# Kernel tuning notes

Hardware: AMD Instinct MI355X
Metric: run time of the kernel (lower is better)

## Reference

```python
import jax, jax.numpy as jnp
import numpy as np
from jax import lax

FORGET_BIAS = 1.0
EPS = 1e-12


def l2_normalize_time(x):
    # tf.nn.l2_normalize(x, dim=1): normalize over the timestep axis
    sq = jnp.sum(jnp.square(x), axis=1, keepdims=True)
    return x * lax.rsqrt(jnp.maximum(sq, EPS))


def lstm_layer(x, W, b, units):
    """TF LSTMCell: kernel (in+units, 4*units), gates split as i, j, f, o.
    x: [B, T, D] -> [B, T, units]"""
    B = x.shape[0]

    def step(carry, xt):
        c, h = carry
        z = jnp.concatenate([xt, h], axis=-1) @ W + b  # [B, 4*units]
        i, j, f, o = jnp.split(z, 4, axis=-1)
        c = jax.nn.sigmoid(f + FORGET_BIAS) * c + jax.nn.sigmoid(i) * jnp.tanh(j)
        h = jax.nn.sigmoid(o) * jnp.tanh(c)
        return (c, h), h

    init = (jnp.zeros((B, units), x.dtype), jnp.zeros((B, units), x.dtype))
    _, hs = lax.scan(step, init, jnp.swapaxes(x, 0, 1))  # [T, B, units]
    return jnp.swapaxes(hs, 0, 1)


def setup_inputs() -> dict:
    key = jax.random.key(0)
    ks = jax.random.split(key, 5)
    B, T, U = 256, 2048, 64
    x = jax.random.normal(ks[0], (B, T, 1), dtype=jnp.float32)
    # layer 0: LSTMCell(64), input dim 1 -> kernel (1+64, 4*64)
    W0 = jax.random.normal(ks[1], (1 + U, 4 * U), dtype=jnp.float32) * 0.05
    b0 = jnp.zeros((4 * U,), dtype=jnp.float32)
    # layer 1: LSTMCell(1), input dim 64 -> kernel (64+1, 4)
    W1 = jax.random.normal(ks[2], (U + 1, 4), dtype=jnp.float32) * 0.05
    b1 = jnp.zeros((4,), dtype=jnp.float32)
    # dense(1)
    Wd = jax.random.normal(ks[3], (1, 1), dtype=jnp.float32)
    bd = jnp.zeros((1,), dtype=jnp.float32)
    return {"x": x, "W0": W0, "b0": b0, "W1": W1, "b1": b1, "Wd": Wd, "bd": bd}


def reference(x, W0, b0, W1, b1, Wd, bd):
    h = l2_normalize_time(x)          # [B, T, 1]
    h = lstm_layer(h, W0, b0, 64)     # [B, T, 64]
    h = lstm_layer(h, W1, b1, 1)      # [B, T, 1]
    out = h @ Wd + bd                 # dense(1), no activation
    return out
```

## Files before the change

### kernel.cpp

```cpp
#include <hip/hip_runtime.h>
#include <math.h>

#define TT 2048
#define UU 64
#define BB 256
#define NTHR 192

typedef float v2f __attribute__((ext_vector_type(2)));
typedef float v4f __attribute__((ext_vector_type(4)));

__device__ __forceinline__ float frcp(float x) { return __builtin_amdgcn_rcpf(x); }
__device__ __forceinline__ float fsigmoid(float x) { return frcp(1.0f + __expf(-x)); }
__device__ __forceinline__ float ftanh(float x) { return 1.0f - 2.0f * frcp(1.0f + __expf(2.0f * x)); }

__device__ __forceinline__ void pkfma(v2f& a, v2f h, v2f w) {
    asm("v_pk_fma_f32 %0, %1, %2, %0" : "+v"(a) : "v"(h), "v"(w));
}

__global__
__attribute__((amdgpu_flat_work_group_size(NTHR, NTHR)))
__attribute__((amdgpu_waves_per_eu(1, 1)))
void lstm_ts_kernel(
    const float* __restrict__ x, const float* __restrict__ W0,
    const float* __restrict__ b0, const float* __restrict__ W1,
    const float* __restrict__ b1, const float* __restrict__ Wd,
    const float* __restrict__ bd, float* __restrict__ out)
{
    __shared__ __align__(16) float xbuf[TT];
    __shared__ __align__(16) float ringS0[2][2 * UU];
    __shared__ __align__(16) float ringS1[2][2 * UU];
    __shared__ __align__(16) v2f zb0[UU];
    __shared__ __align__(16) v2f zb1[UU];
    __shared__ float red[3];

    const int tid = threadIdx.x;
    const int wid = tid >> 6;
    const int u = tid & 63;
    const int b = blockIdx.x;
    const float* xrow = x + b * TT;
    float* outrow = out + b * TT;

    float ss = 0.f;
    for (int i = tid; i < TT; i += NTHR) {
        float v = xrow[i];
        xbuf[i] = v;
        ss += v * v;
    }
    #pragma unroll
    for (int m = 1; m < 64; m <<= 1) ss += __shfl_xor(ss, m, 64);
    if (u == 0) red[wid] = ss;
    if (wid < 2) {
        float* r1 = (wid == 0 ? ringS0 : ringS1)[1];
        r1[2 * u] = 0.f; r1[2 * u + 1] = 0.f;
    }
    __syncthreads();

    if (wid < 2) {
        const int go = wid * 128;
        const float sq = (red[0] + red[1]) + red[2];
        const float scale = 1.0f / sqrtf(fmaxf(sq, 1e-12f));

        #define DECLW(k) v2f WP##k; { const float* r_ = W0 + (1 + (k)) * 256 + go; \
            WP##k.x = r_[u]; WP##k.y = r_[64 + u]; } \
            asm volatile("" : "+v"(WP##k));
        DECLW(0)  DECLW(1)  DECLW(2)  DECLW(3)  DECLW(4)  DECLW(5)  DECLW(6)  DECLW(7)
        DECLW(8)  DECLW(9)  DECLW(10) DECLW(11) DECLW(12) DECLW(13) DECLW(14) DECLW(15)
        DECLW(16) DECLW(17) DECLW(18) DECLW(19) DECLW(20) DECLW(21) DECLW(22) DECLW(23)
        DECLW(24) DECLW(25) DECLW(26) DECLW(27) DECLW(28) DECLW(29) DECLW(30) DECLW(31)
        DECLW(32) DECLW(33) DECLW(34) DECLW(35) DECLW(36) DECLW(37) DECLW(38) DECLW(39)
        DECLW(40) DECLW(41) DECLW(42) DECLW(43) DECLW(44) DECLW(45) DECLW(46) DECLW(47)
        DECLW(48) DECLW(49) DECLW(50) DECLW(51) DECLW(52) DECLW(53) DECLW(54) DECLW(55)
        DECLW(56) DECLW(57) DECLW(58) DECLW(59) DECLW(60) DECLW(61) DECLW(62) DECLW(63)
        #undef DECLW

        const float wxa = W0[go + u] * scale;
        const float wxb = W0[go + 64 + u] * scale;
        const float bca = b0[go + u], bcb = b0[go + 64 + u];

        float (*myring)[2 * UU] = (wid == 0) ? ringS0 : ringS1;
        v2f* zbme = (wid == 0) ? zb0 : zb1;

        float c0 = 0.f;

        for (int t = 0; t < TT; ++t) {
            const float xr = xbuf[t];
            const float* hs = myring[(t + 1) & 1];

            v2f a0, a1 = 0.f, a2 = 0.f, a3 = 0.f;
            a0.x = fmaf(xr, wxa, bca); a0.y = fmaf(xr, wxb, bcb);

            #define MAC2(k2, Wa, Wb, Ae, Ao) { \
                v4f hv_ = *(const v4f*)(hs + 4 * (k2)); \
                v2f hlo_ = __builtin_shufflevector(hv_, hv_, 0, 1); \
                v2f hhi_ = __builtin_shufflevector(hv_, hv_, 2, 3); \
                pkfma(Ae, hlo_, Wa); pkfma(Ao, hhi_, Wb); \
            }
            MAC2(0,  WP0,  WP1,  a0, a1) MAC2(1,  WP2,  WP3,  a2, a3)
            MAC2(2,  WP4,  WP5,  a0, a1) MAC2(3,  WP6,  WP7,  a2, a3)
            MAC2(4,  WP8,  WP9,  a0, a1) MAC2(5,  WP10, WP11, a2, a3)
            MAC2(6,  WP12, WP13, a0, a1) MAC2(7,  WP14, WP15, a2, a3)
            MAC2(8,  WP16, WP17, a0, a1) MAC2(9,  WP18, WP19, a2, a3)
            MAC2(10, WP20, WP21, a0, a1) MAC2(11, WP22, WP23, a2, a3)
            MAC2(12, WP24, WP25, a0, a1) MAC2(13, WP26, WP27, a2, a3)
            MAC2(14, WP28, WP29, a0, a1) MAC2(15, WP30, WP31, a2, a3)
            MAC2(16, WP32, WP33, a0, a1) MAC2(17, WP34, WP35, a2, a3)
            MAC2(18, WP36, WP37, a0, a1) MAC2(19, WP38, WP39, a2, a3)
            MAC2(20, WP40, WP41, a0, a1) MAC2(21, WP42, WP43, a2, a3)
            MAC2(22, WP44, WP45, a0, a1) MAC2(23, WP46, WP47, a2, a3)
            MAC2(24, WP48, WP49, a0, a1) MAC2(25, WP50, WP51, a2, a3)
            MAC2(26, WP52, WP53, a0, a1) MAC2(27, WP54, WP55, a2, a3)
            MAC2(28, WP56, WP57, a0, a1) MAC2(29, WP58, WP59, a2, a3)
            MAC2(30, WP60, WP61, a0, a1) MAC2(31, WP62, WP63, a2, a3)
            #undef MAC2

            zbme[u] = (a0 + a1) + (a2 + a3);
            __syncthreads();

            const v2f zij = zb0[u];
            const v2f zfo = zb1[u];
            c0 = fsigmoid(zfo.x + 1.0f) * c0 + fsigmoid(zij.x) * ftanh(zij.y);
            const float h = fsigmoid(zfo.y) * ftanh(c0);

            v2f hh; hh.x = h; hh.y = h;
            *(v2f*)(&myring[t & 1][2 * u]) = hh;
        }
        __syncthreads();
    } else {
        const float w1v0 = W1[u * 4 + 0], w1v1 = W1[u * 4 + 1];
        const float w1v2 = W1[u * 4 + 2], w1v3 = W1[u * 4 + 3];
        const float w1h0 = W1[256], w1h1 = W1[257], w1h2 = W1[258], w1h3 = W1[259];
        const float b10 = b1[0], b11 = b1[1], b12 = b1[2], b13 = b1[3];
        const float wd = Wd[0], bdv = bd[0];

        float c1 = 0.f, h1 = 0.f, oval = 0.f;

        #define L1STEP(s) { \
            const float hu = ringS0[(s) & 1][2 * u];   \
            float p0 = hu * w1v0, p1 = hu * w1v1, p2 = hu * w1v2, p3 = hu * w1v3; \
            _Pragma("unroll") \
            for (int m = 1; m < 64; m <<= 1) { \
                p0 += __shfl_xor(p0, m, 64); \
                p1 += __shfl_xor(p1, m, 64); \
                p2 += __shfl_xor(p2, m, 64); \
                p3 += __shfl_xor(p3, m, 64); \
            } \
            const float z1i = p0 + fmaf(h1, w1h0, b10); \
            const float z1j = p1 + fmaf(h1, w1h1, b11); \
            const float z1f = p2 + fmaf(h1, w1h2, b12); \
            const float z1o = p3 + fmaf(h1, w1h3, b13); \
            c1 = fsigmoid(z1f + 1.0f) * c1 + fsigmoid(z1i) * ftanh(z1j); \
            h1 = fsigmoid(z1o) * ftanh(c1); \
            const float ov = fmaf(h1, wd, bdv); \
            if (((s) & 63) == u) oval = ov; \
            if (((s) & 63) == 63) outrow[((s) & ~63) + u] = oval; \
        }

        for (int t = 0; t < TT; ++t) {
            __syncthreads();
            if (t > 0) L1STEP(t - 1)
        }
        __syncthreads();
        L1STEP(TT - 1)
        #undef L1STEP
    }
}

extern "C" void kernel_launch(void* const* d_in, const int* in_sizes, int n_in,
                              void* d_out, int out_size, void* d_ws, size_t ws_size,
                              hipStream_t stream) {
    const float* x  = (const float*)d_in[0];
    const float* W0 = (const float*)d_in[1];
    const float* b0 = (const float*)d_in[2];
    const float* W1 = (const float*)d_in[3];
    const float* b1 = (const float*)d_in[4];
    const float* Wd = (const float*)d_in[5];
    const float* bd = (const float*)d_in[6];
    float* out = (float*)d_out;
    lstm_ts_kernel<<<BB, NTHR, 0, stream>>>(x, W0, b0, W1, b1, Wd, bd, out);
}
```

Before: 1.103 ms.

## Move half of recurrent weights to LDS and deepen h ring buffer

Keeps only the first 32 rows of each layer-0 wave's recurrent weights in registers, as 16 v4f. The other 32 rows are staged into a shared-memory array at kernel start and read as v4f every timestep. The h ring grows from two to four slots and the gate-exchange buffer is double-buffered. Each wave also keeps its own gate sums in registers instead of reloading them from shared memory. The aim is to cut register pressure and loosen hazards between the two layer waves, at the cost of 16 extra shared-memory loads per step on the serial recurrence path.

```diff
diff --git a/kernel.cpp b/kernel.cpp
--- a/kernel.cpp
+++ b/kernel.cpp
@@ -27,10 +27,9 @@
     const float* __restrict__ bd, float* __restrict__ out)
 {
     __shared__ __align__(16) float xbuf[TT];
-    __shared__ __align__(16) float ringS0[2][2 * UU];
-    __shared__ __align__(16) float ringS1[2][2 * UU];
-    __shared__ __align__(16) v2f zb0[UU];
-    __shared__ __align__(16) v2f zb1[UU];
+    __shared__ __align__(16) v4f  WL[2][16][UU];
+    __shared__ __align__(16) float ringP[2][4][2 * UU];
+    __shared__ __align__(16) v2f  zb[2][2][UU];
     __shared__ float red[3];
 
     const int tid = threadIdx.x;
@@ -46,12 +45,19 @@
         xbuf[i] = v;
         ss += v * v;
     }
+    for (int idx = tid; idx < 2 * 16 * UU; idx += NTHR) {
+        const int w = idx >> 10, m = (idx >> 6) & 15, uu = idx & 63;
+        const int base = (33 + 2 * m) * 256 + w * 128;
+        v4f e;
+        e.x = W0[base + uu];       e.y = W0[base + 64 + uu];
+        e.z = W0[base + 256 + uu]; e.w = W0[base + 256 + 64 + uu];
+        WL[w][m][uu] = e;
+    }
     #pragma unroll
     for (int m = 1; m < 64; m <<= 1) ss += __shfl_xor(ss, m, 64);
     if (u == 0) red[wid] = ss;
     if (wid < 2) {
-        float* r1 = (wid == 0 ? ringS0 : ringS1)[1];
-        r1[2 * u] = 0.f; r1[2 * u + 1] = 0.f;
+        ringP[wid][3][2 * u] = 0.f; ringP[wid][3][2 * u + 1] = 0.f;
     }
     __syncthreads();
 
@@ -60,69 +66,72 @@
         const float sq = (red[0] + red[1]) + red[2];
         const float scale = 1.0f / sqrtf(fmaxf(sq, 1e-12f));
 
-        #define DECLW(k) v2f WP##k; { const float* r_ = W0 + (1 + (k)) * 256 + go; \
-            WP##k.x = r_[u]; WP##k.y = r_[64 + u]; } \
-            asm volatile("" : "+v"(WP##k));
-        DECLW(0)  DECLW(1)  DECLW(2)  DECLW(3)  DECLW(4)  DECLW(5)  DECLW(6)  DECLW(7)
-        DECLW(8)  DECLW(9)  DECLW(10) DECLW(11) DECLW(12) DECLW(13) DECLW(14) DECLW(15)
-        DECLW(16) DECLW(17) DECLW(18) DECLW(19) DECLW(20) DECLW(21) DECLW(22) DECLW(23)
-        DECLW(24) DECLW(25) DECLW(26) DECLW(27) DECLW(28) DECLW(29) DECLW(30) DECLW(31)
-        DECLW(32) DECLW(33) DECLW(34) DECLW(35) DECLW(36) DECLW(37) DECLW(38) DECLW(39)
-        DECLW(40) DECLW(41) DECLW(42) DECLW(43) DECLW(44) DECLW(45) DECLW(46) DECLW(47)
-        DECLW(48) DECLW(49) DECLW(50) DECLW(51) DECLW(52) DECLW(53) DECLW(54) DECLW(55)
-        DECLW(56) DECLW(57) DECLW(58) DECLW(59) DECLW(60) DECLW(61) DECLW(62) DECLW(63)
-        #undef DECLW
+        #define DECLR(m) v4f R##m; { const float* r_ = W0 + (1 + 2*(m)) * 256 + go; \
+            R##m.x = r_[u]; R##m.y = r_[64 + u]; \
+            R##m.z = r_[256 + u]; R##m.w = r_[256 + 64 + u]; } \
+            asm volatile("" : "+v"(R##m));
+        DECLR(0)  DECLR(1)  DECLR(2)  DECLR(3)  DECLR(4)  DECLR(5)  DECLR(6)  DECLR(7)
+        DECLR(8)  DECLR(9)  DECLR(10) DECLR(11) DECLR(12) DECLR(13) DECLR(14) DECLR(15)
+        #undef DECLR
 
         const float wxa = W0[go + u] * scale;
         const float wxb = W0[go + 64 + u] * scale;
         const float bca = b0[go + u], bcb = b0[go + 64 + u];
 
-        float (*myring)[2 * UU] = (wid == 0) ? ringS0 : ringS1;
-        v2f* zbme = (wid == 0) ? zb0 : zb1;
-
+        float (*myring)[2 * UU] = ringP[wid];
+        const v4f* wl = &WL[wid][0][0];
         float c0 = 0.f;
 
         for (int t = 0; t < TT; ++t) {
             const float xr = xbuf[t];
-            const float* hs = myring[(t + 1) & 1];
+            const float* hs = myring[(t + 3) & 3];
 
             v2f a0, a1 = 0.f, a2 = 0.f, a3 = 0.f;
             a0.x = fmaf(xr, wxa, bca); a0.y = fmaf(xr, wxb, bcb);
 
-            #define MAC2(k2, Wa, Wb, Ae, Ao) { \
+            #define MACR(k2, R, Ae, Ao) { \
                 v4f hv_ = *(const v4f*)(hs + 4 * (k2)); \
                 v2f hlo_ = __builtin_shufflevector(hv_, hv_, 0, 1); \
                 v2f hhi_ = __builtin_shufflevector(hv_, hv_, 2, 3); \
-                pkfma(Ae, hlo_, Wa); pkfma(Ao, hhi_, Wb); \
+                pkfma(Ae, hlo_, __builtin_shufflevector(R, R, 0, 1)); \
+                pkfma(Ao, hhi_, __builtin_shufflevector(R, R, 2, 3)); \
             }
-            MAC2(0,  WP0,  WP1,  a0, a1) MAC2(1,  WP2,  WP3,  a2, a3)
-            MAC2(2,  WP4,  WP5,  a0, a1) MAC2(3,  WP6,  WP7,  a2, a3)
-            MAC2(4,  WP8,  WP9,  a0, a1) MAC2(5,  WP10, WP11, a2, a3)
-            MAC2(6,  WP12, WP13, a0, a1) MAC2(7,  WP14, WP15, a2, a3)
-            MAC2(8,  WP16, WP17, a0, a1) MAC2(9,  WP18, WP19, a2, a3)
-            MAC2(10, WP20, WP21, a0, a1) MAC2(11, WP22, WP23, a2, a3)
-            MAC2(12, WP24, WP25, a0, a1) MAC2(13, WP26, WP27, a2, a3)
-            MAC2(14, WP28, WP29, a0, a1) MAC2(15, WP30, WP31, a2, a3)
-            MAC2(16, WP32, WP33, a0, a1) MAC2(17, WP34, WP35, a2, a3)
-            MAC2(18, WP36, WP37, a0, a1) MAC2(19, WP38, WP39, a2, a3)
-            MAC2(20, WP40, WP41, a0, a1) MAC2(21, WP42, WP43, a2, a3)
-            MAC2(22, WP44, WP45, a0, a1) MAC2(23, WP46, WP47, a2, a3)
-            MAC2(24, WP48, WP49, a0, a1) MAC2(25, WP50, WP51, a2, a3)
-            MAC2(26, WP52, WP53, a0, a1) MAC2(27, WP54, WP55, a2, a3)
-            MAC2(28, WP56, WP57, a0, a1) MAC2(29, WP58, WP59, a2, a3)
-            MAC2(30, WP60, WP61, a0, a1) MAC2(31, WP62, WP63, a2, a3)
-            #undef MAC2
+            #define MACL(k2, Ae, Ao) { \
+                v4f Wv_ = wl[((k2) - 16) * UU + u]; \
+                MACR(k2, Wv_, Ae, Ao) \
+            }
+            MACR(0,  R0,  a0, a1) MACR(1,  R1,  a2, a3)
+            MACR(2,  R2,  a0, a1) MACR(3,  R3,  a2, a3)
+            MACR(4,  R4,  a0, a1) MACR(5,  R5,  a2, a3)
+            MACR(6,  R6,  a0, a1) MACR(7,  R7,  a2, a3)
+            MACR(8,  R8,  a0, a1) MACR(9,  R9,  a2, a3)
+            MACR(10, R10, a0, a1) MACR(11, R11, a2, a3)
+            MACR(12, R12, a0, a1) MACR(13, R13, a2, a3)
+            MACR(14, R14, a0, a1) MACR(15, R15, a2, a3)
+            MACL(16, a0, a1) MACL(17, a2, a3)
+            MACL(18, a0, a1) MACL(19, a2, a3)
+            MACL(20, a0, a1) MACL(21, a2, a3)
+            MACL(22, a0, a1) MACL(23, a2, a3)
+            MACL(24, a0, a1) MACL(25, a2, a3)
+            MACL(26, a0, a1) MACL(27, a2, a3)
+            MACL(28, a0, a1) MACL(29, a2, a3)
+            MACL(30, a0, a1) MACL(31, a2, a3)
+            #undef MACL
+            #undef MACR
 
-            zbme[u] = (a0 + a1) + (a2 + a3);
+            const v2f zown = (a0 + a1) + (a2 + a3);
+            zb[t & 1][wid][u] = zown;
             __syncthreads();
 
-            const v2f zij = zb0[u];
-            const v2f zfo = zb1[u];
+            const v2f zoth = zb[t & 1][1 - wid][u];
+            const v2f zij = (wid == 0) ? zown : zoth;
+            const v2f zfo = (wid == 0) ? zoth : zown;
+
             c0 = fsigmoid(zfo.x + 1.0f) * c0 + fsigmoid(zij.x) * ftanh(zij.y);
             const float h = fsigmoid(zfo.y) * ftanh(c0);
 
             v2f hh; hh.x = h; hh.y = h;
-            *(v2f*)(&myring[t & 1][2 * u]) = hh;
+            *(v2f*)(&myring[t & 3][2 * u]) = hh;
         }
         __syncthreads();
     } else {
@@ -135,7 +144,7 @@
         float c1 = 0.f, h1 = 0.f, oval = 0.f;
 
         #define L1STEP(s) { \
-            const float hu = ringS0[(s) & 1][2 * u];   \
+            const float hu = ringP[0][(s) & 3][2 * u];   \
             float p0 = hu * w1v0, p1 = hu * w1v1, p2 = hu * w1v2, p3 = hu * w1v3; \
             _Pragma("unroll") \
             for (int m = 1; m < 64; m <<= 1) { \
```

Measured after the change: 1.297 ms. 17.6% more time.

## Exchange LSTM gate halves via cross-lane shuffle instead of LDS

Applied to the files above, without the earlier changes.

Layer-0 work is remapped so each wave owns 32 hidden units. The two 32-lane halves of a wave compute the (i,j) and (f,o) gate pairs for the same unit, and they swap partial gate values with a lane-xor-32 shuffle. This removes the per-step LDS write and read of gate pre-activations through the zb buffers from the recurrent critical path, and the two per-wave h rings merge into one shared ring. The layer-1 wave now reads the current step's h right after the same barrier instead of lagging one step, which removes the epilogue step.

```diff
diff --git a/kernel.cpp b/kernel.cpp
--- a/kernel.cpp
+++ b/kernel.cpp
@@ -27,15 +27,12 @@
     const float* __restrict__ bd, float* __restrict__ out)
 {
     __shared__ __align__(16) float xbuf[TT];
-    __shared__ __align__(16) float ringS0[2][2 * UU];
-    __shared__ __align__(16) float ringS1[2][2 * UU];
-    __shared__ __align__(16) v2f zb0[UU];
-    __shared__ __align__(16) v2f zb1[UU];
+    __shared__ __align__(16) float ring[2][2 * UU];
     __shared__ float red[3];
 
     const int tid = threadIdx.x;
     const int wid = tid >> 6;
-    const int u = tid & 63;
+    const int l = tid & 63;
     const int b = blockIdx.x;
     const float* xrow = x + b * TT;
     float* outrow = out + b * TT;
@@ -48,20 +45,20 @@
     }
     #pragma unroll
     for (int m = 1; m < 64; m <<= 1) ss += __shfl_xor(ss, m, 64);
-    if (u == 0) red[wid] = ss;
-    if (wid < 2) {
-        float* r1 = (wid == 0 ? ringS0 : ringS1)[1];
-        r1[2 * u] = 0.f; r1[2 * u + 1] = 0.f;
-    }
+    if (l == 0) red[wid] = ss;
+    if (tid < 2 * UU) ring[1][tid] = 0.f;
     __syncthreads();
 
     if (wid < 2) {
-        const int go = wid * 128;
+        const int p = l >> 5;
+        const int q = l & 31;
+        const int unit = 32 * wid + q;
+        const int go = p * 128;
         const float sq = (red[0] + red[1]) + red[2];
         const float scale = 1.0f / sqrtf(fmaxf(sq, 1e-12f));
 
         #define DECLW(k) v2f WP##k; { const float* r_ = W0 + (1 + (k)) * 256 + go; \
-            WP##k.x = r_[u]; WP##k.y = r_[64 + u]; } \
+            WP##k.x = r_[unit]; WP##k.y = r_[64 + unit]; } \
             asm volatile("" : "+v"(WP##k));
         DECLW(0)  DECLW(1)  DECLW(2)  DECLW(3)  DECLW(4)  DECLW(5)  DECLW(6)  DECLW(7)
         DECLW(8)  DECLW(9)  DECLW(10) DECLW(11) DECLW(12) DECLW(13) DECLW(14) DECLW(15)
@@ -73,18 +70,15 @@
         DECLW(56) DECLW(57) DECLW(58) DECLW(59) DECLW(60) DECLW(61) DECLW(62) DECLW(63)
         #undef DECLW
 
-        const float wxa = W0[go + u] * scale;
-        const float wxb = W0[go + 64 + u] * scale;
-        const float bca = b0[go + u], bcb = b0[go + 64 + u];
-
-        float (*myring)[2 * UU] = (wid == 0) ? ringS0 : ringS1;
-        v2f* zbme = (wid == 0) ? zb0 : zb1;
+        const float wxa = W0[go + unit] * scale;
+        const float wxb = W0[go + 64 + unit] * scale;
+        const float bca = b0[go + unit], bcb = b0[go + 64 + unit];
 
         float c0 = 0.f;
 
         for (int t = 0; t < TT; ++t) {
             const float xr = xbuf[t];
-            const float* hs = myring[(t + 1) & 1];
+            const float* hs = ring[(t + 1) & 1];
 
             v2f a0, a1 = 0.f, a2 = 0.f, a3 = 0.f;
             a0.x = fmaf(xr, wxa, bca); a0.y = fmaf(xr, wxb, bcb);
@@ -113,55 +107,54 @@
             MAC2(30, WP60, WP61, a0, a1) MAC2(31, WP62, WP63, a2, a3)
             #undef MAC2
 
-            zbme[u] = (a0 + a1) + (a2 + a3);
+            const v2f zown = (a0 + a1) + (a2 + a3);
+
+            const float ox = __shfl_xor(zown.x, 32, 64);
+            const float oy = __shfl_xor(zown.y, 32, 64);
+            const float zi = p ? ox : zown.x;
+            const float zj = p ? oy : zown.y;
+            const float zf = p ? zown.x : ox;
+            const float zo = p ? zown.y : oy;
+
+            c0 = fsigmoid(zf + 1.0f) * c0 + fsigmoid(zi) * ftanh(zj);
+            const float h = fsigmoid(zo) * ftanh(c0);
+
+            if (p == 0) {
+                v2f hh; hh.x = h; hh.y = h;
+                *(v2f*)(&ring[t & 1][2 * unit]) = hh;
+            }
             __syncthreads();
-
-            const v2f zij = zb0[u];
-            const v2f zfo = zb1[u];
-            c0 = fsigmoid(zfo.x + 1.0f) * c0 + fsigmoid(zij.x) * ftanh(zij.y);
-            const float h = fsigmoid(zfo.y) * ftanh(c0);
-
-            v2f hh; hh.x = h; hh.y = h;
-            *(v2f*)(&myring[t & 1][2 * u]) = hh;
         }
-        __syncthreads();
     } else {
-        const float w1v0 = W1[u * 4 + 0], w1v1 = W1[u * 4 + 1];
-        const float w1v2 = W1[u * 4 + 2], w1v3 = W1[u * 4 + 3];
+        const float w1v0 = W1[l * 4 + 0], w1v1 = W1[l * 4 + 1];
+        const float w1v2 = W1[l * 4 + 2], w1v3 = W1[l * 4 + 3];
         const float w1h0 = W1[256], w1h1 = W1[257], w1h2 = W1[258], w1h3 = W1[259];
         const float b10 = b1[0], b11 = b1[1], b12 = b1[2], b13 = b1[3];
         const float wd = Wd[0], bdv = bd[0];
 
         float c1 = 0.f, h1 = 0.f, oval = 0.f;
 
-        #define L1STEP(s) { \
-            const float hu = ringS0[(s) & 1][2 * u];   \
-            float p0 = hu * w1v0, p1 = hu * w1v1, p2 = hu * w1v2, p3 = hu * w1v3; \
-            _Pragma("unroll") \
-            for (int m = 1; m < 64; m <<= 1) { \
-                p0 += __shfl_xor(p0, m, 64); \
-                p1 += __shfl_xor(p1, m, 64); \
-                p2 += __shfl_xor(p2, m, 64); \
-                p3 += __shfl_xor(p3, m, 64); \
-            } \
-            const float z1i = p0 + fmaf(h1, w1h0, b10); \
-            const float z1j = p1 + fmaf(h1, w1h1, b11); \
-            const float z1f = p2 + fmaf(h1, w1h2, b12); \
-            const float z1o = p3 + fmaf(h1, w1h3, b13); \
-            c1 = fsigmoid(z1f + 1.0f) * c1 + fsigmoid(z1i) * ftanh(z1j); \
-            h1 = fsigmoid(z1o) * ftanh(c1); \
-            const float ov = fmaf(h1, wd, bdv); \
-            if (((s) & 63) == u) oval = ov; \
-            if (((s) & 63) == 63) outrow[((s) & ~63) + u] = oval; \
-        }
-
         for (int t = 0; t < TT; ++t) {
             __syncthreads();
-            if (t > 0) L1STEP(t - 1)
+            const float hu = ring[t & 1][2 * l];
+            float p0 = hu * w1v0, p1 = hu * w1v1, p2 = hu * w1v2, p3 = hu * w1v3;
+            #pragma unroll
+            for (int m = 1; m < 64; m <<= 1) {
+                p0 += __shfl_xor(p0, m, 64);
+                p1 += __shfl_xor(p1, m, 64);
+                p2 += __shfl_xor(p2, m, 64);
+                p3 += __shfl_xor(p3, m, 64);
+            }
+            const float z1i = p0 + fmaf(h1, w1h0, b10);
+            const float z1j = p1 + fmaf(h1, w1h1, b11);
+            const float z1f = p2 + fmaf(h1, w1h2, b12);
+            const float z1o = p3 + fmaf(h1, w1h3, b13);
+            c1 = fsigmoid(z1f + 1.0f) * c1 + fsigmoid(z1i) * ftanh(z1j);
+            h1 = fsigmoid(z1o) * ftanh(c1);
+            const float ov = fmaf(h1, wd, bdv);
+            if ((t & 63) == l) oval = ov;
+            if ((t & 63) == 63) outrow[(t & ~63) + l] = oval;
         }
-        __syncthreads();
-        L1STEP(TT - 1)
-        #undef L1STEP
     }
 }
 
```

After: 1.677 ms. 52.1% more time.
